# Kernel tuning notes

Measured on AMD Instinct MI355X. Metric: run time of the kernel, lower is better.

Reference implementation:

```python
import jax, jax.numpy as jnp
import numpy as np
from jax import lax

B = 16384
NWIRES = 4


def _conv(x, w, b):
    # NCHW conv, stride 1, SAME padding (pad 1 for k=3)
    y = lax.conv_general_dilated(x, w, (1, 1), ((1, 1), (1, 1)),
                                 dimension_numbers=("NCHW", "OIHW", "NCHW"))
    return y + b[None, :, None, None]


def _pool2(x):
    b, c, h, w = x.shape
    return x.reshape(b, c, h // 2, 2, w // 2, 2).max(axis=(3, 5))


def _apply_1q(state, U, wire):
    # state: (B,2,2,2,2) complex; U: (B,2,2) complex
    s = jnp.moveaxis(state, wire + 1, -1)
    s = jnp.einsum("bij,b...j->b...i", U, s)
    return jnp.moveaxis(s, -1, wire + 1)


def _apply_cnot(state, c, t):
    s0 = jnp.take(state, 0, axis=c + 1)
    s1 = jnp.take(state, 1, axis=c + 1)
    ta = t + 1 if t < c else t  # target axis index after removing control axis
    s1 = jnp.flip(s1, axis=ta)
    return jnp.stack([s0, s1], axis=c + 1)


def _ry(th):
    c = jnp.cos(th / 2)
    s = jnp.sin(th / 2)
    U = jnp.stack([jnp.stack([c, -s], -1), jnp.stack([s, c], -1)], -2)
    return U.astype(jnp.complex64)


def _rz(th):
    e = jnp.exp(-0.5j * th.astype(jnp.complex64))
    z = jnp.zeros_like(e)
    return jnp.stack([jnp.stack([e, z], -1), jnp.stack([z, jnp.conj(e)], -1)], -2)


def _rx(th):
    c = jnp.cos(th / 2).astype(jnp.complex64)
    s = jnp.sin(th / 2).astype(jnp.complex64)
    return jnp.stack([jnp.stack([c, -1j * s], -1), jnp.stack([-1j * s, c], -1)], -2)


def _circuit(params):
    # params: (B, 16) -> PauliZ expvals (B, 4)
    b = params.shape[0]
    state = jnp.zeros((b, 16), jnp.complex64).at[:, 0].set(1.0).reshape(b, 2, 2, 2, 2)
    for i in range(NWIRES):
        state = _apply_1q(state, _ry(params[:, 4 * i + 0]), i)
        state = _apply_1q(state, _rz(params[:, 4 * i + 1]), i)
        state = _apply_1q(state, _rx(params[:, 4 * i + 2]), i)
        state = _apply_cnot(state, i, (i + 1) % NWIRES)
    probs = state.real ** 2 + state.imag ** 2  # (B,2,2,2,2)
    zs = []
    for i in range(NWIRES):
        p = probs.sum(axis=tuple(a for a in range(1, 5) if a != i + 1))  # (B,2)
        zs.append(p[:, 0] - p[:, 1])
    return jnp.stack(zs, axis=-1)


def setup_inputs() -> dict:
    key = jax.random.key(0)
    ks = jax.random.split(key, 12)
    d = {}
    d["x"] = jax.random.normal(ks[0], (B, 1, 28, 28), jnp.float32)
    d["conv1_w"] = jax.random.normal(ks[1], (4, 1, 3, 3), jnp.float32) * 0.3
    d["conv1_b"] = jax.random.normal(ks[2], (4,), jnp.float32) * 0.1
    d["conv2_w"] = jax.random.normal(ks[3], (4, 4, 3, 3), jnp.float32) * 0.15
    d["conv2_b"] = jax.random.normal(ks[4], (4,), jnp.float32) * 0.1
    d["pl_w"] = jax.random.normal(ks[5], (16, 196), jnp.float32) * 0.07
    d["pl_b"] = jax.random.normal(ks[6], (16,), jnp.float32) * 0.05
    d["ro_w"] = jax.random.normal(ks[7], (4, 4), jnp.float32) * 0.5
    d["ro_b"] = jax.random.normal(ks[8], (4,), jnp.float32) * 0.1
    d["bn_w"] = jnp.ones((4,), jnp.float32)
    d["bn_b"] = jnp.zeros((4,), jnp.float32)
    return d


def reference(x, conv1_w, conv1_b, conv2_w, conv2_b, pl_w, pl_b, ro_w, ro_b, bn_w, bn_b):
    h = _pool2(jax.nn.relu(_conv(x, conv1_w, conv1_b)))   # (B,4,14,14)
    h = _pool2(jax.nn.relu(_conv(h, conv2_w, conv2_b)))   # (B,4,7,7)
    flat = h.reshape(x.shape[0], -1)                      # (B,196)
    params = flat @ pl_w.T + pl_b                         # (B,16)
    z = _circuit(params)                                  # (B,4)
    out = z @ ro_w.T + ro_b                               # (B,4)
    mean = out.mean(0)
    var = out.var(0)  # biased, matches torch BN training normalization
    return (out - mean) / jnp.sqrt(var + 1e-5) * bn_w + bn_b
```

## Files before the change

kernel.cpp:

```cpp
#include <hip/hip_runtime.h>
#include <math.h>

#define BATCH 16384

typedef float v2f __attribute__((ext_vector_type(2)));

__device__ __forceinline__ v2f pk_fma(v2f a, v2f b, v2f c) {
  return __builtin_elementwise_fma(a, b, c);
}
__device__ __forceinline__ v2f pk_max(v2f a, v2f b) {
  return __builtin_elementwise_max(a, b);
}

__device__ __forceinline__ unsigned bf2(float lo, float hi) {
  unsigned a = __float_as_uint(lo);
  unsigned b = __float_as_uint(hi);
  a = (a + 0x7fffu + ((a >> 16) & 1u)) >> 16;
  b = (b + 0x7fffu + ((b >> 16) & 1u)) & 0xffff0000u;
  return a | b;
}

__global__ __launch_bounds__(256) void qnat_fused(
    const float* __restrict__ x,
    const float* __restrict__ w1,
    const float* __restrict__ b1,
    const float* __restrict__ w2,
    const float* __restrict__ b2,
    const float* __restrict__ plw,
    const float* __restrict__ plb,
    const float* __restrict__ rw,
    const float* __restrict__ rb,
    float* __restrict__ pre,
    float* __restrict__ stats)
{
  __shared__ __align__(16) float h1p[4][4 * 288 + 16];
  __shared__ __align__(16) float h2[4][4][200];
  __shared__ __align__(16) uint4 plw_tb[25 * 16];
  __shared__ float s_red[4][8];

  const int tid = threadIdx.x;
  const int w = tid >> 6;
  const int lane = tid & 63;
  const int base = (blockIdx.x * 4 + w) * 4;

  #pragma unroll
  for (int j = 0; j < 2; j++) {
    int s = tid + 256 * j;
    if (s < 400) {
      int tp = s >> 4;
      int k = s & 15;
      const float4* pr = (const float4*)(plw + k * 196);
      float4 a = pr[2 * tp];
      float4 b = (tp < 24) ? pr[2 * tp + 1] : make_float4(0.f, 0.f, 0.f, 0.f);
      plw_tb[s] = make_uint4(bf2(a.x, a.y), bf2(a.z, a.w),
                             bf2(b.x, b.y), bf2(b.z, b.w));
    }
  }

  {
    float4 z4 = make_float4(0.f, 0.f, 0.f, 0.f);
    float4* hz = (float4*)&h1p[w][0];
    #pragma unroll
    for (int t = 0; t < 5; t++) {
      int p = t * 64 + lane;
      if (p < 292) hz[p] = z4;
    }
    if (lane < 16) h2[w][lane >> 2][196 + (lane & 3)] = 0.0f;
  }
  __syncthreads();

  const int i = lane >> 2;
  const int q = lane & 3;
  const bool c1act = lane < 56;

  float4 pfa[4], pfb[4];
  float pe0[4], pe1[4];
  #pragma unroll
  for (int r = 0; r < 4; r++) {
    pfa[r] = make_float4(0,0,0,0); pfb[r] = make_float4(0,0,0,0);
    pe0[r] = 0.0f; pe1[r] = 0.0f;
  }

  if (c1act) {
    const float* xb = x + (size_t)base * 784;
    #pragma unroll
    for (int r = 0; r < 4; r++) {
      int row = 2 * i - 1 + r;
      if (0 <= row && row < 28) {
        const float* rp = xb + row * 28;
        pfa[r] = *(const float4*)(rp + 8 * q);
        if (q > 0) pe0[r] = rp[8 * q - 1];
        if (q < 3) {
          pfb[r] = *(const float4*)(rp + 8 * q + 4);
          pe1[r] = rp[8 * q + 8];
        }
      }
    }
  }

  for (int it = 0; it < 4; ++it) {
    if (c1act) {
      float win[4][10];
      #pragma unroll
      for (int r = 0; r < 4; r++) {
        win[r][0] = pe0[r];
        win[r][1] = pfa[r].x; win[r][2] = pfa[r].y;
        win[r][3] = pfa[r].z; win[r][4] = pfa[r].w;
        win[r][5] = pfb[r].x; win[r][6] = pfb[r].y;
        win[r][7] = pfb[r].z; win[r][8] = pfb[r].w;
        win[r][9] = pe1[r];
      }
      if (it != 3) {
        const float* xn = x + (size_t)(base + it + 1) * 784;
        #pragma unroll
        for (int r = 0; r < 4; r++) {
          int row = 2 * i - 1 + r;
          pfa[r] = make_float4(0,0,0,0);
          pfb[r] = make_float4(0,0,0,0);
          pe0[r] = 0.0f; pe1[r] = 0.0f;
          if (0 <= row && row < 28) {
            const float* rp = xn + row * 28;
            pfa[r] = *(const float4*)(rp + 8 * q);
            if (q > 0) pe0[r] = rp[8 * q - 1];
            if (q < 3) {
              pfb[r] = *(const float4*)(rp + 8 * q + 4);
              pe1[r] = rp[8 * q + 8];
            }
          }
        }
      }
      v2f P[4][9];
      #pragma unroll
      for (int r = 0; r < 4; r++)
        #pragma unroll
        for (int k = 0; k < 9; k++) P[r][k] = (v2f){win[r][k], win[r][k + 1]};

      float* hb = &h1p[w][18 * (i + 1) + 1 + 4 * q];
      #pragma unroll
      for (int c = 0; c < 4; c++) {
        const float* wc = w1 + c * 9;
        const v2f bias2 = (v2f){b1[c], b1[c]};
        v2f a0[4], a1[4];
        #pragma unroll
        for (int jj = 0; jj < 4; jj++) { a0[jj] = bias2; a1[jj] = bias2; }
        #pragma unroll
        for (int dy = 0; dy < 3; dy++)
          #pragma unroll
          for (int dx = 0; dx < 3; dx++) {
            const float wv = wc[dy * 3 + dx];
            const v2f wvv = (v2f){wv, wv};
            #pragma unroll
            for (int jj = 0; jj < 4; jj++) {
              a0[jj] = pk_fma(P[dy][2 * jj + dx],     wvv, a0[jj]);
              a1[jj] = pk_fma(P[dy + 1][2 * jj + dx], wvv, a1[jj]);
            }
          }
        float m[4];
        #pragma unroll
        for (int jj = 0; jj < 4; jj++) {
          v2f mm = pk_max(a0[jj], a1[jj]);
          m[jj] = fmaxf(fmaxf(mm.x, mm.y), 0.0f);
        }
        float* p = hb + 288 * c;
        if (q < 3) {
          p[0] = m[0];
          *(float2*)(p + 1) = make_float2(m[1], m[2]);
          p[3] = m[3];
        } else {
          p[0] = m[0];
          p[1] = m[1];
        }
      }
    }

    {
      const int jq = lane & 7;
      const int i2 = lane >> 3;
      if (i2 < 7 && jq < 7) {
        v2f acc[4][2];
        #pragma unroll
        for (int co = 0; co < 4; co++) {
          const v2f bb = (v2f){b2[co], b2[co]};
          acc[co][0] = bb; acc[co][1] = bb;
        }
        #pragma unroll
        for (int ci = 0; ci < 4; ci++) {
          const float* rp = &h1p[w][288 * ci + 36 * i2 + 2 * jq];
          v2f Q[4][3];
          #pragma unroll
          for (int r = 0; r < 4; r++) {
            v2f a = *(const v2f*)(rp + 18 * r);
            v2f b = *(const v2f*)(rp + 18 * r + 2);
            Q[r][0] = a;
            Q[r][1] = (v2f){a.y, b.x};
            Q[r][2] = b;
          }
          #pragma unroll
          for (int co = 0; co < 4; co++) {
            const float* wp = w2 + (co * 4 + ci) * 9;
            #pragma unroll
            for (int dy = 0; dy < 3; dy++)
              #pragma unroll
              for (int dx = 0; dx < 3; dx++) {
                const float wv = wp[dy * 3 + dx];
                const v2f wvv = (v2f){wv, wv};
                acc[co][0] = pk_fma(Q[dy][dx],     wvv, acc[co][0]);
                acc[co][1] = pk_fma(Q[dy + 1][dx], wvv, acc[co][1]);
              }
          }
        }
        #pragma unroll
        for (int co = 0; co < 4; co++) {
          v2f mm = pk_max(acc[co][0], acc[co][1]);
          h2[w][it][49 * co + 7 * i2 + jq] = fmaxf(fmaxf(mm.x, mm.y), 0.0f);
        }
      }
    }
  }

  const int s2 = lane >> 4;
  const int k = lane & 15;

  float cv, sv;
  {
    const float4* hv4 = (const float4*)&h2[w][s2][0];
    const uint4*  wb4 = &plw_tb[k];
    v2f sacc = (v2f){0.0f, 0.0f};
    #pragma unroll
    for (int t = 0; t < 25; t++) {
      float4 h0 = hv4[2 * t];
      float4 h1 = hv4[2 * t + 1];
      uint4 wb = wb4[16 * t];
      v2f w01 = (v2f){__uint_as_float(wb.x << 16), __uint_as_float(wb.x & 0xffff0000u)};
      v2f w23 = (v2f){__uint_as_float(wb.y << 16), __uint_as_float(wb.y & 0xffff0000u)};
      v2f w45 = (v2f){__uint_as_float(wb.z << 16), __uint_as_float(wb.z & 0xffff0000u)};
      v2f w67 = (v2f){__uint_as_float(wb.w << 16), __uint_as_float(wb.w & 0xffff0000u)};
      sacc = pk_fma((v2f){h0.x, h0.y}, w01, sacc);
      sacc = pk_fma((v2f){h0.z, h0.w}, w23, sacc);
      sacc = pk_fma((v2f){h1.x, h1.y}, w45, sacc);
      sacc = pk_fma((v2f){h1.z, h1.w}, w67, sacc);
    }
    float pv = sacc.x + sacc.y + plb[k];
    __sincosf(pv * 0.5f, &sv, &cv);
  }

  {
    const int l = k;
    const int gb = lane & 48;
    float re = (l == 0) ? 1.0f : 0.0f;
    float im = 0.0f;
    #pragma unroll
    for (int qi = 0; qi < 4; qi++) {
      const int beta = 3 - qi;
      const int m = 1 << beta;
      const int b = (l >> beta) & 1;
      float c = __shfl(cv, gb + 4 * qi, 64), s = __shfl(sv, gb + 4 * qi, 64);
      float pr_ = __shfl_xor(re, m, 64), pi_ = __shfl_xor(im, m, 64);
      float sg = b ? s : -s;
      re = fmaf(c, re, sg * pr_);
      im = fmaf(c, im, sg * pi_);
      c = __shfl(cv, gb + 4 * qi + 1, 64); s = __shfl(sv, gb + 4 * qi + 1, 64);
      float sz = b ? s : -s;
      float nr = c * re - sz * im;
      float ni = c * im + sz * re;
      re = nr; im = ni;
      c = __shfl(cv, gb + 4 * qi + 2, 64); s = __shfl(sv, gb + 4 * qi + 2, 64);
      pr_ = __shfl_xor(re, m, 64); pi_ = __shfl_xor(im, m, 64);
      nr = fmaf(c, re, s * pi_);
      ni = fmaf(c, im, -s * pr_);
      re = nr; im = ni;
      const int tm = 1 << (3 - ((qi + 1) & 3));
      float fr = __shfl_xor(re, tm, 64), fi = __shfl_xor(im, tm, 64);
      if (b) { re = fr; im = fi; }
    }
    float pr2 = re * re + im * im;
    float z0 = ((l >> 3) & 1) ? -pr2 : pr2;
    float z1 = ((l >> 2) & 1) ? -pr2 : pr2;
    float z2 = ((l >> 1) & 1) ? -pr2 : pr2;
    float z3 = (l & 1) ? -pr2 : pr2;
    #pragma unroll
    for (int off = 8; off >= 1; off >>= 1) {
      z0 += __shfl_xor(z0, off, 64);
      z1 += __shfl_xor(z1, off, 64);
      z2 += __shfl_xor(z2, off, 64);
      z3 += __shfl_xor(z3, off, 64);
    }
    float as0 = 0.f, as1 = 0.f, as2 = 0.f, as3 = 0.f;
    float aq0 = 0.f, aq1 = 0.f, aq2 = 0.f, aq3 = 0.f;
    if (l == 0) {
      float o0 = fmaf(rw[0],  z0, fmaf(rw[1],  z1, fmaf(rw[2],  z2, fmaf(rw[3],  z3, rb[0]))));
      float o1 = fmaf(rw[4],  z0, fmaf(rw[5],  z1, fmaf(rw[6],  z2, fmaf(rw[7],  z3, rb[1]))));
      float o2 = fmaf(rw[8],  z0, fmaf(rw[9],  z1, fmaf(rw[10], z2, fmaf(rw[11], z3, rb[2]))));
      float o3 = fmaf(rw[12], z0, fmaf(rw[13], z1, fmaf(rw[14], z2, fmaf(rw[15], z3, rb[3]))));
      *(float4*)(pre + (size_t)(base + s2) * 4) = make_float4(o0, o1, o2, o3);
      as0 = o0; aq0 = o0 * o0;
      as1 = o1; aq1 = o1 * o1;
      as2 = o2; aq2 = o2 * o2;
      as3 = o3; aq3 = o3 * o3;
    }
    #pragma unroll
    for (int off = 32; off >= 16; off >>= 1) {
      as0 += __shfl_down(as0, off, 64); aq0 += __shfl_down(aq0, off, 64);
      as1 += __shfl_down(as1, off, 64); aq1 += __shfl_down(aq1, off, 64);
      as2 += __shfl_down(as2, off, 64); aq2 += __shfl_down(aq2, off, 64);
      as3 += __shfl_down(as3, off, 64); aq3 += __shfl_down(aq3, off, 64);
    }
    if (lane == 0) {
      s_red[w][0] = as0; s_red[w][4] = aq0;
      s_red[w][1] = as1; s_red[w][5] = aq1;
      s_red[w][2] = as2; s_red[w][6] = aq2;
      s_red[w][3] = as3; s_red[w][7] = aq3;
    }
  }
  __syncthreads();
  if (tid < 8) {
    float v = s_red[0][tid] + s_red[1][tid] + s_red[2][tid] + s_red[3][tid];
    atomicAdd(&stats[tid], v);
  }
}

__global__ __launch_bounds__(256) void qnat_bn(
    float* __restrict__ pre,
    const float* __restrict__ stats,
    const float* __restrict__ bnw,
    const float* __restrict__ bnb)
{
  int idx = blockIdx.x * 256 + threadIdx.x;
  int c = idx & 3;
  float mean = stats[c] * (1.0f / BATCH);
  float ex2 = stats[4 + c] * (1.0f / BATCH);
  float var = ex2 - mean * mean;
  float inv = rsqrtf(var + 1e-5f);
  pre[idx] = (pre[idx] - mean) * inv * bnw[c] + bnb[c];
}

extern "C" void kernel_launch(void* const* d_in, const int* in_sizes, int n_in,
                              void* d_out, int out_size, void* d_ws, size_t ws_size,
                              hipStream_t stream) {
  const float* x   = (const float*)d_in[0];
  const float* w1  = (const float*)d_in[1];
  const float* b1  = (const float*)d_in[2];
  const float* w2  = (const float*)d_in[3];
  const float* b2  = (const float*)d_in[4];
  const float* plw = (const float*)d_in[5];
  const float* plb = (const float*)d_in[6];
  const float* rw  = (const float*)d_in[7];
  const float* rb  = (const float*)d_in[8];
  const float* bnw = (const float*)d_in[9];
  const float* bnb = (const float*)d_in[10];

  float* out   = (float*)d_out;
  float* stats = (float*)d_ws;

  hipMemsetAsync(stats, 0, 8 * sizeof(float), stream);
  qnat_fused<<<BATCH / 16, 256, 0, stream>>>(x, w1, b1, w2, b2, plw, plb, rw, rb, out, stats);
  qnat_bn<<<(BATCH * 4) / 256, 256, 0, stream>>>(out, stats, bnw, bnb);
}
```

Baseline: 133.4 us.

## Halve samples per wave, double grid, shuffle halo loads, bf16 pooled features

Each wave now handles two samples instead of four, and the grid is doubled, which shortens each wave's serial loop and raises parallelism. The launch bound now requests 8 blocks per CU. Horizontal halo pixels are taken from neighbouring lanes with shuffles instead of extra scalar global loads. The pooled conv2 output is stored as bf16 so the linear-layer dot product can be split across both wave halves and combined with a shuffle. The cost is lower precision on the projected features and duplicated per-block weight staging across twice as many blocks.

```diff
diff --git a/kernel.cpp b/kernel.cpp
--- a/kernel.cpp
+++ b/kernel.cpp
@@ -19,8 +19,13 @@
   b = (b + 0x7fffu + ((b >> 16) & 1u)) & 0xffff0000u;
   return a | b;
 }
-
-__global__ __launch_bounds__(256) void qnat_fused(
+__device__ __forceinline__ unsigned short bf1(float v) {
+  unsigned u = __float_as_uint(v);
+  u = (u + 0x7fffu + ((u >> 16) & 1u)) >> 16;
+  return (unsigned short)u;
+}
+
+__global__ __launch_bounds__(256, 8) void qnat_fused(
     const float* __restrict__ x,
     const float* __restrict__ w1,
     const float* __restrict__ b1,
@@ -34,14 +39,14 @@
     float* __restrict__ stats)
 {
   __shared__ __align__(16) float h1p[4][4 * 288 + 16];
-  __shared__ __align__(16) float h2[4][4][200];
+  __shared__ __align__(16) unsigned short h2[4][2][200];
   __shared__ __align__(16) uint4 plw_tb[25 * 16];
   __shared__ float s_red[4][8];
 
   const int tid = threadIdx.x;
   const int w = tid >> 6;
   const int lane = tid & 63;
-  const int base = (blockIdx.x * 4 + w) * 4;
+  const int base = (blockIdx.x * 4 + w) * 2;
 
   #pragma unroll
   for (int j = 0; j < 2; j++) {
@@ -65,7 +70,7 @@
       int p = t * 64 + lane;
       if (p < 292) hz[p] = z4;
     }
-    if (lane < 16) h2[w][lane >> 2][196 + (lane & 3)] = 0.0f;
+    if (lane < 4) ((unsigned*)&h2[w][lane >> 1][196])[lane & 1] = 0u;
   }
   __syncthreads();
 
@@ -74,12 +79,8 @@
   const bool c1act = lane < 56;
 
   float4 pfa[4], pfb[4];
-  float pe0[4], pe1[4];
   #pragma unroll
-  for (int r = 0; r < 4; r++) {
-    pfa[r] = make_float4(0,0,0,0); pfb[r] = make_float4(0,0,0,0);
-    pe0[r] = 0.0f; pe1[r] = 0.0f;
-  }
+  for (int r = 0; r < 4; r++) { pfa[r] = make_float4(0,0,0,0); pfb[r] = make_float4(0,0,0,0); }
 
   if (c1act) {
     const float* xb = x + (size_t)base * 784;
@@ -89,86 +90,87 @@
       if (0 <= row && row < 28) {
         const float* rp = xb + row * 28;
         pfa[r] = *(const float4*)(rp + 8 * q);
-        if (q > 0) pe0[r] = rp[8 * q - 1];
-        if (q < 3) {
-          pfb[r] = *(const float4*)(rp + 8 * q + 4);
-          pe1[r] = rp[8 * q + 8];
-        }
-      }
-    }
-  }
-
-  for (int it = 0; it < 4; ++it) {
-    if (c1act) {
-      float win[4][10];
+        if (q < 3) pfb[r] = *(const float4*)(rp + 8 * q + 4);
+      }
+    }
+  }
+
+  #pragma unroll
+  for (int it = 0; it < 2; ++it) {
+    {
+      float hl[4], hr[4];
       #pragma unroll
       for (int r = 0; r < 4; r++) {
-        win[r][0] = pe0[r];
-        win[r][1] = pfa[r].x; win[r][2] = pfa[r].y;
-        win[r][3] = pfa[r].z; win[r][4] = pfa[r].w;
-        win[r][5] = pfb[r].x; win[r][6] = pfb[r].y;
-        win[r][7] = pfb[r].z; win[r][8] = pfb[r].w;
-        win[r][9] = pe1[r];
-      }
-      if (it != 3) {
-        const float* xn = x + (size_t)(base + it + 1) * 784;
+        float left = __shfl_up(pfb[r].w, 1, 64);
+        hl[r] = (q == 0) ? 0.0f : left;
+        hr[r] = __shfl_down(pfa[r].x, 1, 64);
+      }
+      if (c1act) {
+        float win[4][10];
         #pragma unroll
         for (int r = 0; r < 4; r++) {
-          int row = 2 * i - 1 + r;
-          pfa[r] = make_float4(0,0,0,0);
-          pfb[r] = make_float4(0,0,0,0);
-          pe0[r] = 0.0f; pe1[r] = 0.0f;
-          if (0 <= row && row < 28) {
-            const float* rp = xn + row * 28;
-            pfa[r] = *(const float4*)(rp + 8 * q);
-            if (q > 0) pe0[r] = rp[8 * q - 1];
-            if (q < 3) {
-              pfb[r] = *(const float4*)(rp + 8 * q + 4);
-              pe1[r] = rp[8 * q + 8];
+          win[r][0] = hl[r];
+          win[r][1] = pfa[r].x; win[r][2] = pfa[r].y;
+          win[r][3] = pfa[r].z; win[r][4] = pfa[r].w;
+          win[r][5] = pfb[r].x; win[r][6] = pfb[r].y;
+          win[r][7] = pfb[r].z; win[r][8] = pfb[r].w;
+          win[r][9] = hr[r];
+        }
+        if (it == 0) {
+          const float* xn = x + (size_t)(base + 1) * 784;
+          #pragma unroll
+          for (int r = 0; r < 4; r++) {
+            int row = 2 * i - 1 + r;
+            pfa[r] = make_float4(0,0,0,0);
+            pfb[r] = make_float4(0,0,0,0);
+            if (0 <= row && row < 28) {
+              const float* rp = xn + row * 28;
+              pfa[r] = *(const float4*)(rp + 8 * q);
+              if (q < 3) pfb[r] = *(const float4*)(rp + 8 * q + 4);
             }
           }
         }
-      }
-      v2f P[4][9];
-      #pragma unroll
-      for (int r = 0; r < 4; r++)
-        #pragma unroll
-        for (int k = 0; k < 9; k++) P[r][k] = (v2f){win[r][k], win[r][k + 1]};
-
-      float* hb = &h1p[w][18 * (i + 1) + 1 + 4 * q];
-      #pragma unroll
-      for (int c = 0; c < 4; c++) {
-        const float* wc = w1 + c * 9;
-        const v2f bias2 = (v2f){b1[c], b1[c]};
-        v2f a0[4], a1[4];
-        #pragma unroll
-        for (int jj = 0; jj < 4; jj++) { a0[jj] = bias2; a1[jj] = bias2; }
-        #pragma unroll
-        for (int dy = 0; dy < 3; dy++)
-          #pragma unroll
-          for (int dx = 0; dx < 3; dx++) {
-            const float wv = wc[dy * 3 + dx];
-            const v2f wvv = (v2f){wv, wv};
+        v2f P[4][9];
+        #pragma unroll
+        for (int r = 0; r < 4; r++)
+          #pragma unroll
+          for (int k = 0; k < 9; k++) P[r][k] = (v2f){win[r][k], win[r][k + 1]};
+
+        float* hb = &h1p[w][18 * (i + 1) + 1 + 4 * q];
+        #pragma unroll
+        for (int c = 0; c < 4; c++) {
+          const float* wc = w1 + c * 9;
+          const v2f bias2 = (v2f){b1[c], b1[c]};
+          v2f a0[4], a1[4];
+          #pragma unroll
+          for (int jj = 0; jj < 4; jj++) { a0[jj] = bias2; a1[jj] = bias2; }
+          #pragma unroll
+          for (int dy = 0; dy < 3; dy++)
             #pragma unroll
-            for (int jj = 0; jj < 4; jj++) {
-              a0[jj] = pk_fma(P[dy][2 * jj + dx],     wvv, a0[jj]);
-              a1[jj] = pk_fma(P[dy + 1][2 * jj + dx], wvv, a1[jj]);
+            for (int dx = 0; dx < 3; dx++) {
+              const float wv = wc[dy * 3 + dx];
+              const v2f wvv = (v2f){wv, wv};
+              #pragma unroll
+              for (int jj = 0; jj < 4; jj++) {
+                a0[jj] = pk_fma(P[dy][2 * jj + dx],     wvv, a0[jj]);
+                a1[jj] = pk_fma(P[dy + 1][2 * jj + dx], wvv, a1[jj]);
+              }
             }
-          }
-        float m[4];
-        #pragma unroll
-        for (int jj = 0; jj < 4; jj++) {
-          v2f mm = pk_max(a0[jj], a1[jj]);
-          m[jj] = fmaxf(fmaxf(mm.x, mm.y), 0.0f);
-        }
-        float* p = hb + 288 * c;
-        if (q < 3) {
-          p[0] = m[0];
-          *(float2*)(p + 1) = make_float2(m[1], m[2]);
-          p[3] = m[3];
-        } else {
-          p[0] = m[0];
-          p[1] = m[1];
+          float m[4];
+          #pragma unroll
+          for (int jj = 0; jj < 4; jj++) {
+            v2f mm = pk_max(a0[jj], a1[jj]);
+            m[jj] = fmaxf(fmaxf(mm.x, mm.y), 0.0f);
+          }
+          float* p = hb + 288 * c;
+          if (q < 3) {
+            p[0] = m[0];
+            *(float2*)(p + 1) = make_float2(m[1], m[2]);
+            p[3] = m[3];
+          } else {
+            p[0] = m[0];
+            p[1] = m[1];
+          }
         }
       }
     }
@@ -212,35 +214,44 @@
         #pragma unroll
         for (int co = 0; co < 4; co++) {
           v2f mm = pk_max(acc[co][0], acc[co][1]);
-          h2[w][it][49 * co + 7 * i2 + jq] = fmaxf(fmaxf(mm.x, mm.y), 0.0f);
-        }
-      }
-    }
-  }
-
-  const int s2 = lane >> 4;
+          h2[w][it][49 * co + 7 * i2 + jq] = bf1(fmaxf(fmaxf(mm.x, mm.y), 0.0f));
+        }
+      }
+    }
+  }
+
+  const int half = lane >> 5;
+  const int s2 = (lane >> 4) & 1;
   const int k = lane & 15;
 
   float cv, sv;
   {
-    const float4* hv4 = (const float4*)&h2[w][s2][0];
-    const uint4*  wb4 = &plw_tb[k];
+    const uint4* hv4 = (const uint4*)&h2[w][s2][0];
+    const uint4* wb4 = &plw_tb[k];
     v2f sacc = (v2f){0.0f, 0.0f};
     #pragma unroll
-    for (int t = 0; t < 25; t++) {
-      float4 h0 = hv4[2 * t];
-      float4 h1 = hv4[2 * t + 1];
-      uint4 wb = wb4[16 * t];
-      v2f w01 = (v2f){__uint_as_float(wb.x << 16), __uint_as_float(wb.x & 0xffff0000u)};
-      v2f w23 = (v2f){__uint_as_float(wb.y << 16), __uint_as_float(wb.y & 0xffff0000u)};
-      v2f w45 = (v2f){__uint_as_float(wb.z << 16), __uint_as_float(wb.z & 0xffff0000u)};
-      v2f w67 = (v2f){__uint_as_float(wb.w << 16), __uint_as_float(wb.w & 0xffff0000u)};
-      sacc = pk_fma((v2f){h0.x, h0.y}, w01, sacc);
-      sacc = pk_fma((v2f){h0.z, h0.w}, w23, sacc);
-      sacc = pk_fma((v2f){h1.x, h1.y}, w45, sacc);
-      sacc = pk_fma((v2f){h1.z, h1.w}, w67, sacc);
-    }
-    float pv = sacc.x + sacc.y + plb[k];
+    for (int t = 0; t < 13; t++) {
+      if (half | (t < 12)) {
+        int tt = half ? (12 + t) : t;
+        uint4 hb = hv4[tt];
+        uint4 wb = wb4[16 * tt];
+        v2f h01 = (v2f){__uint_as_float(hb.x << 16), __uint_as_float(hb.x & 0xffff0000u)};
+        v2f h23 = (v2f){__uint_as_float(hb.y << 16), __uint_as_float(hb.y & 0xffff0000u)};
+        v2f h45 = (v2f){__uint_as_float(hb.z << 16), __uint_as_float(hb.z & 0xffff0000u)};
+        v2f h67 = (v2f){__uint_as_float(hb.w << 16), __uint_as_float(hb.w & 0xffff0000u)};
+        v2f w01 = (v2f){__uint_as_float(wb.x << 16), __uint_as_float(wb.x & 0xffff0000u)};
+        v2f w23 = (v2f){__uint_as_float(wb.y << 16), __uint_as_float(wb.y & 0xffff0000u)};
+        v2f w45 = (v2f){__uint_as_float(wb.z << 16), __uint_as_float(wb.z & 0xffff0000u)};
+        v2f w67 = (v2f){__uint_as_float(wb.w << 16), __uint_as_float(wb.w & 0xffff0000u)};
+        sacc = pk_fma(h01, w01, sacc);
+        sacc = pk_fma(h23, w23, sacc);
+        sacc = pk_fma(h45, w45, sacc);
+        sacc = pk_fma(h67, w67, sacc);
+      }
+    }
+    float s = sacc.x + sacc.y;
+    s += __shfl_xor(s, 32, 64);
+    float pv = s + plb[k];
     __sincosf(pv * 0.5f, &sv, &cv);
   }
 
@@ -287,7 +298,7 @@
     }
     float as0 = 0.f, as1 = 0.f, as2 = 0.f, as3 = 0.f;
     float aq0 = 0.f, aq1 = 0.f, aq2 = 0.f, aq3 = 0.f;
-    if (l == 0) {
+    if (l == 0 && half == 0) {
       float o0 = fmaf(rw[0],  z0, fmaf(rw[1],  z1, fmaf(rw[2],  z2, fmaf(rw[3],  z3, rb[0]))));
       float o1 = fmaf(rw[4],  z0, fmaf(rw[5],  z1, fmaf(rw[6],  z2, fmaf(rw[7],  z3, rb[1]))));
       float o2 = fmaf(rw[8],  z0, fmaf(rw[9],  z1, fmaf(rw[10], z2, fmaf(rw[11], z3, rb[2]))));
@@ -298,13 +309,10 @@
       as2 = o2; aq2 = o2 * o2;
       as3 = o3; aq3 = o3 * o3;
     }
-    #pragma unroll
-    for (int off = 32; off >= 16; off >>= 1) {
-      as0 += __shfl_down(as0, off, 64); aq0 += __shfl_down(aq0, off, 64);
-      as1 += __shfl_down(as1, off, 64); aq1 += __shfl_down(aq1, off, 64);
-      as2 += __shfl_down(as2, off, 64); aq2 += __shfl_down(aq2, off, 64);
-      as3 += __shfl_down(as3, off, 64); aq3 += __shfl_down(aq3, off, 64);
-    }
+    as0 += __shfl_down(as0, 16, 64); aq0 += __shfl_down(aq0, 16, 64);
+    as1 += __shfl_down(as1, 16, 64); aq1 += __shfl_down(aq1, 16, 64);
+    as2 += __shfl_down(as2, 16, 64); aq2 += __shfl_down(aq2, 16, 64);
+    as3 += __shfl_down(as3, 16, 64); aq3 += __shfl_down(aq3, 16, 64);
     if (lane == 0) {
       s_red[w][0] = as0; s_red[w][4] = aq0;
       s_red[w][1] = as1; s_red[w][5] = aq1;
@@ -353,6 +361,6 @@
   float* stats = (float*)d_ws;
 
   hipMemsetAsync(stats, 0, 8 * sizeof(float), stream);
-  qnat_fused<<<BATCH / 16, 256, 0, stream>>>(x, w1, b1, w2, b2, plw, plb, rw, rb, out, stats);
+  qnat_fused<<<BATCH / 8, 256, 0, stream>>>(x, w1, b1, w2, b2, plw, plb, rw, rb, out, stats);
   qnat_bn<<<(BATCH * 4) / 256, 256, 0, stream>>>(out, stats, bnw, bnb);
 }
```

Measured after the change: 144.3 us. 1.08x slower.
